# Kernel optimization log

Measured on AMD Instinct MI355X. Metric: run time of the kernel, lower is better.

## Reference

```python
import jax, jax.numpy as jnp
import numpy as np

N_NODES = 50000
N_EDGES = 600000
IN_DIM, HID_DIM, OUT_DIM = 128, 256, 40


def setup_inputs() -> dict:
    key = jax.random.key(0)
    ks = jax.random.split(key, 10)
    x = jax.random.normal(ks[0], (N_NODES, IN_DIM), dtype=jnp.float32)
    edge_index = jax.random.randint(ks[1], (2, N_EDGES), 0, N_NODES, dtype=jnp.int64)
    def lin(k, out_d, in_d):
        s = 1.0 / np.sqrt(in_d)
        return jax.random.uniform(k, (out_d, in_d), jnp.float32, -s, s)
    # SAGEConv: lin_l (on aggregated neighbors, with bias) + lin_r (on self, no bias)
    params = {
        "Wl1": lin(ks[2], HID_DIM, IN_DIM), "bl1": jnp.zeros((HID_DIM,), jnp.float32), "Wr1": lin(ks[3], HID_DIM, IN_DIM),
        "Wl2": lin(ks[4], HID_DIM, HID_DIM), "bl2": jnp.zeros((HID_DIM,), jnp.float32), "Wr2": lin(ks[5], HID_DIM, HID_DIM),
        "Wl3": lin(ks[6], OUT_DIM, HID_DIM), "bl3": jnp.zeros((OUT_DIM,), jnp.float32), "Wr3": lin(ks[7], OUT_DIM, HID_DIM),
    }
    return {"x": x, "edge_index": edge_index, **params}


def _sage_conv(x, src, dst, Wl, bl, Wr):
    # mean-aggregate source features into destination nodes
    n = x.shape[0]
    agg = jax.ops.segment_sum(x[src], dst, num_segments=n)          # [N, d_in]
    cnt = jax.ops.segment_sum(jnp.ones_like(dst, dtype=x.dtype), dst, num_segments=n)
    mean = agg / jnp.maximum(cnt, 1.0)[:, None]
    return mean @ Wl.T + bl + x @ Wr.T


def reference(x, edge_index, Wl1, bl1, Wr1, Wl2, bl2, Wr2, Wl3, bl3, Wr3):
    src, dst = edge_index[0], edge_index[1]
    h = _sage_conv(x, src, dst, Wl1, bl1, Wr1)
    h = jax.nn.relu(h)  # dropout is identity in eval mode
    h = _sage_conv(h, src, dst, Wl2, bl2, Wr2)
    h = jax.nn.relu(h)
    h = _sage_conv(h, src, dst, Wl3, bl3, Wr3)
    return jax.nn.log_softmax(h, axis=1)
```

## Files before the change

kernel.cpp:

```cpp
#include <hip/hip_runtime.h>
#include <hip/hip_bf16.h>

#define IN_DIM 128
#define HID_DIM 256
#define OUT_DIM 40
#define SCAN_CHUNK 2048

typedef __attribute__((ext_vector_type(8))) __bf16 bf16x8;
typedef __attribute__((ext_vector_type(4))) float f32x4;

__device__ inline ushort f2bf(float f) {
    uint u = __builtin_bit_cast(uint, f);
    u = (u + 0x7fff + ((u >> 16) & 1)) >> 16;
    return (ushort)u;
}
__device__ inline float bfl(uint u) { return __builtin_bit_cast(float, u << 16); }
__device__ inline float bfh(uint u) { return __builtin_bit_cast(float, u & 0xffff0000u); }

__global__ __launch_bounds__(256) void prep_kernel(
    const float* __restrict__ x, ushort* __restrict__ xb, int n4, int XB,
    const float* __restrict__ Wl1, const float* __restrict__ Wr1,
    const float* __restrict__ Wl2, const float* __restrict__ Wr2,
    const float* __restrict__ Wl3, const float* __restrict__ Wr3,
    ushort* __restrict__ o1l, ushort* __restrict__ o1r,
    ushort* __restrict__ o2l, ushort* __restrict__ o2r,
    ushort* __restrict__ o3l, ushort* __restrict__ o3r, int WB,
    const int* __restrict__ dst, int* __restrict__ cnt, int E) {
    int b = blockIdx.x;
    if (b < XB) {
        int i = b * 256 + threadIdx.x;
        if (i < n4) {
            float4 v = ((const float4*)x)[i];
            uint2 o;
            o.x = (uint)f2bf(v.x) | ((uint)f2bf(v.y) << 16);
            o.y = (uint)f2bf(v.z) | ((uint)f2bf(v.w) << 16);
            ((uint2*)xb)[i] = o;
        }
        return;
    }
    b -= XB;
    if (b < WB) {
        int idx = b * 256 + threadIdx.x;
        if (idx < 32768) {
            o1l[idx] = f2bf(Wl1[idx]);
            o1r[idx] = f2bf(Wr1[idx]);
            return;
        }
        idx -= 32768;
        if (idx < 65536) {
            o2l[idx] = f2bf(Wl2[idx]);
            o2r[idx] = f2bf(Wr2[idx]);
            return;
        }
        idx -= 65536;
        if (idx < 48 * 256) {
            int row = idx >> 8;
            int col = idx & 255;
            ushort vl = 0, vr = 0;
            if (row < OUT_DIM) {
                vl = f2bf(Wl3[row * 256 + col]);
                vr = f2bf(Wr3[row * 256 + col]);
            }
            o3l[idx] = vl;
            o3r[idx] = vr;
        }
        return;
    }
    b -= WB;
    int e = b * 256 + threadIdx.x;
    if (e < E) atomicAdd(&cnt[dst[e]], 1);
}

__global__ __launch_bounds__(256) void scan_pass1(const int* __restrict__ cnt,
                                                  int* __restrict__ bsum, int N) {
    __shared__ int red[256];
    const int base = blockIdx.x * SCAN_CHUNK;
    int s = 0;
    for (int i = threadIdx.x; i < SCAN_CHUNK; i += 256) {
        int idx = base + i;
        if (idx < N) s += cnt[idx];
    }
    red[threadIdx.x] = s;
    __syncthreads();
    for (int o = 128; o > 0; o >>= 1) {
        if (threadIdx.x < o) red[threadIdx.x] += red[threadIdx.x + o];
        __syncthreads();
    }
    if (threadIdx.x == 0) bsum[blockIdx.x] = red[0];
}

__global__ __launch_bounds__(256) void scan_pass3(const int* __restrict__ cnt,
                                                  const int* __restrict__ bsum,
                                                  int* __restrict__ rowptr,
                                                  int* __restrict__ cursor,
                                                  float* __restrict__ inv,
                                                  int N, int E, int SB) {
    __shared__ int ls[256];
    __shared__ int boff;
    if (threadIdx.x == 0) {
        int r = 0;
        for (int i = 0; i < blockIdx.x; ++i) r += bsum[i];
        boff = r;
    }
    const int tbase = blockIdx.x * SCAN_CHUNK + threadIdx.x * 8;
    int c[8];
    int s = 0;
#pragma unroll
    for (int j = 0; j < 8; ++j) {
        int idx = tbase + j;
        c[j] = (idx < N) ? cnt[idx] : 0;
        s += c[j];
    }
    ls[threadIdx.x] = s;
    __syncthreads();
    for (int o = 1; o < 256; o <<= 1) {
        int u = (threadIdx.x >= o) ? ls[threadIdx.x - o] : 0;
        __syncthreads();
        ls[threadIdx.x] += u;
        __syncthreads();
    }
    int run = boff + ls[threadIdx.x] - s;
#pragma unroll
    for (int j = 0; j < 8; ++j) {
        int idx = tbase + j;
        if (idx < N) {
            rowptr[idx] = run;
            cursor[idx] = run;
            inv[idx] = 1.0f / fmaxf((float)c[j], 1.0f);
            run += c[j];
        }
    }
    if (blockIdx.x == 0 && threadIdx.x == 0) rowptr[N] = E;
}

__global__ __launch_bounds__(256) void fill_kernel(const int* __restrict__ src,
                                                   const int* __restrict__ dst,
                                                   int* __restrict__ cursor,
                                                   int* __restrict__ srcs, int E) {
    int e = blockIdx.x * 256 + threadIdx.x;
    if (e < E) {
        int pos = atomicAdd(&cursor[dst[e]], 1);
        srcs[pos] = src[e];
    }
}

template <int D>
__global__ __launch_bounds__(256) void gather_mean_bf(const ushort* __restrict__ feat,
                                                      const int* __restrict__ rowptr,
                                                      const int* __restrict__ srcs,
                                                      const float* __restrict__ inv,
                                                      ushort* __restrict__ out, int N) {
    constexpr int V = D / 64;
    const int wave = threadIdx.x >> 6;
    const int lane = threadIdx.x & 63;
    const int n = blockIdx.x * 4 + wave;
    if (n >= N) return;
    const int beg = rowptr[n];
    const int end = rowptr[n + 1];
    const int col = lane * V;
    float a0 = 0.f, a1 = 0.f, a2 = 0.f, a3 = 0.f;
    int e = beg;
    if constexpr (V == 4) {
        for (; e + 7 < end; e += 8) {
            uint2 q[8];
#pragma unroll
            for (int j = 0; j < 8; ++j)
                q[j] = *(const uint2*)&feat[(long long)srcs[e + j] * D + col];
#pragma unroll
            for (int j = 0; j < 8; ++j) {
                a0 += bfl(q[j].x); a1 += bfh(q[j].x);
                a2 += bfl(q[j].y); a3 += bfh(q[j].y);
            }
        }
        for (; e + 3 < end; e += 4) {
            uint2 q[4];
#pragma unroll
            for (int j = 0; j < 4; ++j)
                q[j] = *(const uint2*)&feat[(long long)srcs[e + j] * D + col];
#pragma unroll
            for (int j = 0; j < 4; ++j) {
                a0 += bfl(q[j].x); a1 += bfh(q[j].x);
                a2 += bfl(q[j].y); a3 += bfh(q[j].y);
            }
        }
        for (; e < end; ++e) {
            uint2 q0 = *(const uint2*)&feat[(long long)srcs[e] * D + col];
            a0 += bfl(q0.x); a1 += bfh(q0.x); a2 += bfl(q0.y); a3 += bfh(q0.y);
        }
        const float sc = inv[n];
        uint2 o;
        o.x = (uint)f2bf(a0 * sc) | ((uint)f2bf(a1 * sc) << 16);
        o.y = (uint)f2bf(a2 * sc) | ((uint)f2bf(a3 * sc) << 16);
        *(uint2*)&out[(long long)n * D + col] = o;
    } else {
        for (; e + 7 < end; e += 8) {
            uint q[8];
#pragma unroll
            for (int j = 0; j < 8; ++j)
                q[j] = *(const uint*)&feat[(long long)srcs[e + j] * D + col];
#pragma unroll
            for (int j = 0; j < 8; ++j) {
                a0 += bfl(q[j]); a1 += bfh(q[j]);
            }
        }
        for (; e + 3 < end; e += 4) {
            uint q[4];
#pragma unroll
            for (int j = 0; j < 4; ++j)
                q[j] = *(const uint*)&feat[(long long)srcs[e + j] * D + col];
#pragma unroll
            for (int j = 0; j < 4; ++j) {
                a0 += bfl(q[j]); a1 += bfh(q[j]);
            }
        }
        for (; e < end; ++e) {
            uint q0 = *(const uint*)&feat[(long long)srcs[e] * D + col];
            a0 += bfl(q0); a1 += bfh(q0);
        }
        const float sc = inv[n];
        uint o = (uint)f2bf(a0 * sc) | ((uint)f2bf(a1 * sc) << 16);
        *(uint*)&out[(long long)n * D + col] = o;
    }
}

template <int K, bool RELU, bool OUTBF>
__global__ __launch_bounds__(256, 3) void sage_gemm_mfma(const ushort* __restrict__ Amean,
                                                         const ushort* __restrict__ Aself,
                                                         const ushort* __restrict__ Wl,
                                                         const float* __restrict__ bias,
                                                         const ushort* __restrict__ Wr,
                                                         void* __restrict__ outv, int N, int O) {
    constexpr int KP = K + 8;
    constexpr int NK = K / 32;
    __shared__ __align__(16) ushort Ws[64 * KP];

    const int tid = threadIdx.x;
    const int wave = tid >> 6;
    const int lane = tid & 63;
    const int ln = lane & 15;
    const int quad = lane >> 4;
    const int bm0 = blockIdx.y * 128;
    const int bn0 = blockIdx.x * 64;

    int arow[2];
#pragma unroll
    for (int rt = 0; rt < 2; ++rt) {
        int r = bm0 + wave * 32 + rt * 16 + ln;
        arow[rt] = min(r, N - 1);
    }

    f32x4 acc[2][4] = {};

    for (int phase = 0; phase < 2; ++phase) {
        const ushort* __restrict__ A = phase ? Aself : Amean;
        const ushort* __restrict__ W = phase ? Wr : Wl;

        __syncthreads();
#pragma unroll
        for (int i = tid; i < 64 * (K / 8); i += 256) {
            int row = i / (K / 8);
            int c8 = (i % (K / 8)) * 8;
            *(ulonglong2*)&Ws[row * KP + c8] =
                *(const ulonglong2*)&W[(long long)(bn0 + row) * K + c8];
        }
        __syncthreads();

        bf16x8 areg[NK][2];
#pragma unroll
        for (int kk = 0; kk < NK; ++kk)
#pragma unroll
            for (int rt = 0; rt < 2; ++rt)
                areg[kk][rt] = *(const bf16x8*)&A[(long long)arow[rt] * K + kk * 32 + quad * 8];

#pragma unroll
        for (int kk = 0; kk < NK; ++kk) {
#pragma unroll
            for (int ct = 0; ct < 4; ++ct) {
                bf16x8 b = *(const bf16x8*)&Ws[(ct * 16 + ln) * KP + kk * 32 + quad * 8];
#pragma unroll
                for (int rt = 0; rt < 2; ++rt)
                    acc[rt][ct] = __builtin_amdgcn_mfma_f32_16x16x32_bf16(areg[kk][rt], b, acc[rt][ct], 0, 0, 0);
            }
        }
    }

#pragma unroll
    for (int rt = 0; rt < 2; ++rt) {
        int rbase = bm0 + wave * 32 + rt * 16 + quad * 4;
#pragma unroll
        for (int ct = 0; ct < 4; ++ct) {
            int col = bn0 + ct * 16 + ln;
            if (col >= O) continue;
            float bv = bias[col];
#pragma unroll
            for (int r = 0; r < 4; ++r) {
                int row = rbase + r;
                if (row >= N) continue;
                float v = acc[rt][ct][r] + bv;
                if (RELU) v = fmaxf(v, 0.f);
                if (OUTBF)
                    ((ushort*)outv)[(long long)row * O + col] = f2bf(v);
                else
                    ((float*)outv)[(long long)row * O + col] = v;
            }
        }
    }
}

template <int K>
__global__ __launch_bounds__(256, 3) void sage_gemm_pre(const ushort* __restrict__ A0,
                                                        const ushort* __restrict__ Wl,
                                                        const ushort* __restrict__ Wr,
                                                        ushort* __restrict__ P,
                                                        float* __restrict__ S, int N, int O) {
    constexpr int KP = 2 * K + 8;
    constexpr int NK = K / 32;
    __shared__ __align__(16) ushort Ws[48 * KP];

    const int tid = threadIdx.x;
    const int wave = tid >> 6;
    const int lane = tid & 63;
    const int ln = lane & 15;
    const int quad = lane >> 4;
    const int bm0 = blockIdx.x * 64;

    const int arow = min(bm0 + wave * 16 + ln, N - 1);

#pragma unroll
    for (int i = tid; i < 48 * (K / 8); i += 256) {
        int row = i / (K / 8);
        int c8 = (i % (K / 8)) * 8;
        *(ulonglong2*)&Ws[row * KP + c8] =
            *(const ulonglong2*)&Wl[(long long)row * K + c8];
        *(ulonglong2*)&Ws[row * KP + K + c8] =
            *(const ulonglong2*)&Wr[(long long)row * K + c8];
    }
    __syncthreads();

#pragma unroll
    for (int phase = 0; phase < 2; ++phase) {
        f32x4 acc[3] = {};
#pragma unroll
        for (int kk = 0; kk < NK; ++kk) {
            bf16x8 a = *(const bf16x8*)&A0[(long long)arow * K + kk * 32 + quad * 8];
#pragma unroll
            for (int ct = 0; ct < 3; ++ct) {
                bf16x8 b = *(const bf16x8*)&Ws[(ct * 16 + ln) * KP + phase * K + kk * 32 + quad * 8];
                acc[ct] = __builtin_amdgcn_mfma_f32_16x16x32_bf16(a, b, acc[ct], 0, 0, 0);
            }
        }
        int rbase = bm0 + wave * 16 + quad * 4;
#pragma unroll
        for (int ct = 0; ct < 3; ++ct) {
            int col = ct * 16 + ln;
            if (col >= O) continue;
#pragma unroll
            for (int r = 0; r < 4; ++r) {
                int row = rbase + r;
                if (row >= N) continue;
                if (phase == 0)
                    P[(long long)row * O + col] = f2bf(acc[ct][r]);
                else
                    S[(long long)row * O + col] = acc[ct][r];
            }
        }
    }
}

__global__ __launch_bounds__(256) void agg_bias_lsm(const ushort* __restrict__ P,
                                                    const float* __restrict__ S,
                                                    const float* __restrict__ bias,
                                                    const int* __restrict__ rowptr,
                                                    const int* __restrict__ srcs,
                                                    const float* __restrict__ inv,
                                                    float* __restrict__ out, int N) {
    const int wave = threadIdx.x >> 6;
    const int lane = threadIdx.x & 63;
    const int n = blockIdx.x * 4 + wave;
    if (n >= N) return;
    const int beg = rowptr[n];
    const int end = rowptr[n + 1];
    const bool act = lane < OUT_DIM;
    const int cidx = act ? lane : 0;

    float acc = 0.f;
    int e = beg;
    for (; e + 3 < end; e += 4) {
        int s0 = srcs[e], s1 = srcs[e + 1], s2 = srcs[e + 2], s3 = srcs[e + 3];
        float v0 = __builtin_bit_cast(float, (uint)P[(long long)s0 * OUT_DIM + cidx] << 16);
        float v1 = __builtin_bit_cast(float, (uint)P[(long long)s1 * OUT_DIM + cidx] << 16);
        float v2 = __builtin_bit_cast(float, (uint)P[(long long)s2 * OUT_DIM + cidx] << 16);
        float v3 = __builtin_bit_cast(float, (uint)P[(long long)s3 * OUT_DIM + cidx] << 16);
        acc += (v0 + v1) + (v2 + v3);
    }
    for (; e < end; ++e)
        acc += __builtin_bit_cast(float, (uint)P[(long long)srcs[e] * OUT_DIM + cidx] << 16);

    float v = act ? (acc * inv[n] + S[(long long)n * OUT_DIM + lane] + bias[lane]) : -INFINITY;
    float m = v;
#pragma unroll
    for (int o = 32; o > 0; o >>= 1) m = fmaxf(m, __shfl_xor(m, o, 64));
    float ex = act ? expf(v - m) : 0.f;
    float sm = ex;
#pragma unroll
    for (int o = 32; o > 0; o >>= 1) sm += __shfl_xor(sm, o, 64);
    float ls = logf(sm);
    if (act) out[(long long)n * OUT_DIM + lane] = v - m - ls;
}

extern "C" void kernel_launch(void* const* d_in, const int* in_sizes, int n_in,
                              void* d_out, int out_size, void* d_ws, size_t ws_size,
                              hipStream_t stream) {
    const float* x   = (const float*)d_in[0];
    const int*   ei  = (const int*)d_in[1];
    const float* Wl1 = (const float*)d_in[2];
    const float* bl1 = (const float*)d_in[3];
    const float* Wr1 = (const float*)d_in[4];
    const float* Wl2 = (const float*)d_in[5];
    const float* bl2 = (const float*)d_in[6];
    const float* Wr2 = (const float*)d_in[7];
    const float* Wl3 = (const float*)d_in[8];
    const float* bl3 = (const float*)d_in[9];
    const float* Wr3 = (const float*)d_in[10];
    float* out = (float*)d_out;

    const int N = in_sizes[0] / IN_DIM;
    const int E = in_sizes[1] / 2;
    const int* src = ei;
    const int* dst = ei + E;

    char* w = (char*)d_ws;
    size_t off = 0;
    auto alloc = [&](size_t bytes) {
        void* p = w + off;
        off = (off + bytes + 255) & ~(size_t)255;
        return p;
    };
    ushort* xb   = (ushort*)alloc((size_t)N * IN_DIM * 2);
    ushort* M    = (ushort*)alloc((size_t)N * HID_DIM * 2);
    ushort* H1   = (ushort*)alloc((size_t)N * HID_DIM * 2);
    ushort* H2   = (ushort*)alloc((size_t)N * HID_DIM * 2);
    ushort* P3   = (ushort*)alloc((size_t)N * OUT_DIM * 2);
    float*  S3   = (float*)alloc((size_t)N * OUT_DIM * 4);
    float*  inv  = (float*)alloc((size_t)N * 4);
    int*    cnt  = (int*)alloc((size_t)N * 4);
    int*    rowptr = (int*)alloc((size_t)(N + 1) * 4);
    int*    cursor = (int*)alloc((size_t)N * 4);
    int*    srcs = (int*)alloc((size_t)E * 4);
    int*    bsum = (int*)alloc(256 * 4);
    ushort* Wl1b = (ushort*)alloc(256 * 128 * 2);
    ushort* Wr1b = (ushort*)alloc(256 * 128 * 2);
    ushort* Wl2b = (ushort*)alloc(256 * 256 * 2);
    ushort* Wr2b = (ushort*)alloc(256 * 256 * 2);
    ushort* Wl3b = (ushort*)alloc(48 * 256 * 2);
    ushort* Wr3b = (ushort*)alloc(48 * 256 * 2);

    const int n4 = N * IN_DIM / 4;
    const int XB = (n4 + 255) / 256;
    const int WB = (32768 + 65536 + 48 * 256 + 255) / 256;
    const int HB = (E + 255) / 256;
    hipMemsetAsync(cnt, 0, (size_t)N * sizeof(int), stream);
    prep_kernel<<<XB + WB + HB, 256, 0, stream>>>(
        x, xb, n4, XB,
        Wl1, Wr1, Wl2, Wr2, Wl3, Wr3,
        Wl1b, Wr1b, Wl2b, Wr2b, Wl3b, Wr3b, WB,
        dst, cnt, E);

    const int SB = (N + SCAN_CHUNK - 1) / SCAN_CHUNK;
    scan_pass1<<<SB, 256, 0, stream>>>(cnt, bsum, N);
    scan_pass3<<<SB, 256, 0, stream>>>(cnt, bsum, rowptr, cursor, inv, N, E, SB);
    fill_kernel<<<HB, 256, 0, stream>>>(src, dst, cursor, srcs, E);

    const int gm = (N + 127) / 128;
    const int gg = (N + 3) / 4;

    gather_mean_bf<IN_DIM><<<gg, 256, 0, stream>>>(xb, rowptr, srcs, inv, M, N);
    sage_gemm_mfma<IN_DIM, true, true><<<dim3(4, gm), 256, 0, stream>>>(
        M, xb, Wl1b, bl1, Wr1b, H1, N, HID_DIM);

    gather_mean_bf<HID_DIM><<<gg, 256, 0, stream>>>(H1, rowptr, srcs, inv, M, N);
    sage_gemm_mfma<HID_DIM, true, true><<<dim3(4, gm), 256, 0, stream>>>(
        M, H1, Wl2b, bl2, Wr2b, H2, N, HID_DIM);

    sage_gemm_pre<HID_DIM><<<(N + 63) / 64, 256, 0, stream>>>(
        H2, Wl3b, Wr3b, P3, S3, N, OUT_DIM);
    agg_bias_lsm<<<gg, 256, 0, stream>>>(P3, S3, bl3, rowptr, srcs, inv, out, N);
}
```

Measured before the change: 354.6 us.

## Pre-swizzle weights into MFMA fragment order and async-load both tiles into LDS

The prep kernel now writes layer-1 and layer-2 bf16 weights in an order matching the MFMA B-fragment layout. The GEMM then loads both the Wl and Wr tiles straight from global memory into LDS with global_load_lds, and reads them with contiguous, conflict-free fragment reads. All A fragments for both phases are loaded up front, so the two-phase loop needs one barrier instead of four, and loads can overlap. In exchange the kernel uses twice the LDS and more registers, so the occupancy hint drops from 3 to 2 blocks per SM.

```diff
diff --git a/kernel.cpp b/kernel.cpp
--- a/kernel.cpp
+++ b/kernel.cpp
@@ -16,6 +16,11 @@
 }
 __device__ inline float bfl(uint u) { return __builtin_bit_cast(float, u << 16); }
 __device__ inline float bfh(uint u) { return __builtin_bit_cast(float, u & 0xffff0000u); }
+
+__device__ inline void gload_lds16(const ushort* g, ushort* l) {
+    __builtin_amdgcn_global_load_lds((const __attribute__((address_space(1))) void*)g,
+                                     (__attribute__((address_space(3))) void*)l, 16, 0, 0);
+}
 
 __global__ __launch_bounds__(256) void prep_kernel(
     const float* __restrict__ x, ushort* __restrict__ xb, int n4, int XB,
@@ -42,14 +47,22 @@
     if (b < WB) {
         int idx = b * 256 + threadIdx.x;
         if (idx < 32768) {
-            o1l[idx] = f2bf(Wl1[idx]);
-            o1r[idx] = f2bf(Wr1[idx]);
+            int j = idx & 7, ln = (idx >> 3) & 15, quad = (idx >> 7) & 3;
+            int kk = (idx >> 9) & 3, ct = (idx >> 11) & 3, cb = idx >> 13;
+            int o = cb * 64 + ct * 16 + ln;
+            int k = kk * 32 + quad * 8 + j;
+            o1l[idx] = f2bf(Wl1[o * 128 + k]);
+            o1r[idx] = f2bf(Wr1[o * 128 + k]);
             return;
         }
         idx -= 32768;
         if (idx < 65536) {
-            o2l[idx] = f2bf(Wl2[idx]);
-            o2r[idx] = f2bf(Wr2[idx]);
+            int j = idx & 7, ln = (idx >> 3) & 15, quad = (idx >> 7) & 3;
+            int kk = (idx >> 9) & 7, ct = (idx >> 12) & 3, cb = idx >> 14;
+            int o = cb * 64 + ct * 16 + ln;
+            int k = kk * 32 + quad * 8 + j;
+            o2l[idx] = f2bf(Wl2[o * 256 + k]);
+            o2r[idx] = f2bf(Wr2[o * 256 + k]);
             return;
         }
         idx -= 65536;
@@ -224,15 +237,16 @@
 }
 
 template <int K, bool RELU, bool OUTBF>
-__global__ __launch_bounds__(256, 3) void sage_gemm_mfma(const ushort* __restrict__ Amean,
+__global__ __launch_bounds__(256, 2) void sage_gemm_mfma(const ushort* __restrict__ Amean,
                                                          const ushort* __restrict__ Aself,
                                                          const ushort* __restrict__ Wl,
                                                          const float* __restrict__ bias,
                                                          const ushort* __restrict__ Wr,
                                                          void* __restrict__ outv, int N, int O) {
-    constexpr int KP = K + 8;
     constexpr int NK = K / 32;
-    __shared__ __align__(16) ushort Ws[64 * KP];
+    constexpr int TILE = 64 * K;
+    constexpr int CHUNKS = TILE / 512;
+    __shared__ __align__(16) ushort Ws[2 * TILE];
 
     const int tid = threadIdx.x;
     const int wave = tid >> 6;
@@ -240,7 +254,15 @@
     const int ln = lane & 15;
     const int quad = lane >> 4;
     const int bm0 = blockIdx.y * 128;
-    const int bn0 = blockIdx.x * 64;
+    const int cb = blockIdx.x;
+
+#pragma unroll
+    for (int p = 0; p < 2; ++p) {
+        const ushort* gsrc = (p ? Wr : Wl) + (size_t)cb * TILE;
+#pragma unroll
+        for (int c = wave; c < CHUNKS; c += 4)
+            gload_lds16(gsrc + c * 512 + lane * 8, &Ws[p * TILE + c * 512]);
+    }
 
     int arow[2];
 #pragma unroll
@@ -249,37 +271,30 @@
         arow[rt] = min(r, N - 1);
     }
 
+    bf16x8 areg[2][NK][2];
+#pragma unroll
+    for (int p = 0; p < 2; ++p) {
+        const ushort* __restrict__ A = p ? Aself : Amean;
+#pragma unroll
+        for (int kk = 0; kk < NK; ++kk)
+#pragma unroll
+            for (int rt = 0; rt < 2; ++rt)
+                areg[p][kk][rt] = *(const bf16x8*)&A[(long long)arow[rt] * K + kk * 32 + quad * 8];
+    }
+
     f32x4 acc[2][4] = {};
-
-    for (int phase = 0; phase < 2; ++phase) {
-        const ushort* __restrict__ A = phase ? Aself : Amean;
-        const ushort* __restrict__ W = phase ? Wr : Wl;
-
-        __syncthreads();
-#pragma unroll
-        for (int i = tid; i < 64 * (K / 8); i += 256) {
-            int row = i / (K / 8);
-            int c8 = (i % (K / 8)) * 8;
-            *(ulonglong2*)&Ws[row * KP + c8] =
-                *(const ulonglong2*)&W[(long long)(bn0 + row) * K + c8];
-        }
-        __syncthreads();
-
-        bf16x8 areg[NK][2];
-#pragma unroll
-        for (int kk = 0; kk < NK; ++kk)
-#pragma unroll
-            for (int rt = 0; rt < 2; ++rt)
-                areg[kk][rt] = *(const bf16x8*)&A[(long long)arow[rt] * K + kk * 32 + quad * 8];
-
+    __syncthreads();
+
+#pragma unroll
+    for (int p = 0; p < 2; ++p) {
 #pragma unroll
         for (int kk = 0; kk < NK; ++kk) {
 #pragma unroll
             for (int ct = 0; ct < 4; ++ct) {
-                bf16x8 b = *(const bf16x8*)&Ws[(ct * 16 + ln) * KP + kk * 32 + quad * 8];
+                bf16x8 b = *(const bf16x8*)&Ws[p * TILE + ((ct * NK + kk) * 64 + lane) * 8];
 #pragma unroll
                 for (int rt = 0; rt < 2; ++rt)
-                    acc[rt][ct] = __builtin_amdgcn_mfma_f32_16x16x32_bf16(areg[kk][rt], b, acc[rt][ct], 0, 0, 0);
+                    acc[rt][ct] = __builtin_amdgcn_mfma_f32_16x16x32_bf16(areg[p][kk][rt], b, acc[rt][ct], 0, 0, 0);
             }
         }
     }
@@ -289,7 +304,7 @@
         int rbase = bm0 + wave * 32 + rt * 16 + quad * 4;
 #pragma unroll
         for (int ct = 0; ct < 4; ++ct) {
-            int col = bn0 + ct * 16 + ln;
+            int col = cb * 64 + ct * 16 + ln;
             if (col >= O) continue;
             float bv = bias[col];
 #pragma unroll
```

New measurement: 361.0 us. Within noise of the previous version (+1.8%).
